# Kernel tuning notes

Hardware: AMD Instinct MI355X
Metric: run time of the kernel (lower is better)

Reference implementation:

```python
import jax, jax.numpy as jnp
import numpy as np

D = 1024
H = 16
HD = D // H
EPS = 1e-5

def _ln(t, gamma, beta):
    # LayerNorm over last dim (head_dim)
    mu = jnp.mean(t, axis=-1, keepdims=True)
    var = jnp.mean(jnp.square(t - mu), axis=-1, keepdims=True)
    return (t - mu) * jax.lax.rsqrt(var + EPS) * gamma + beta

def setup_inputs() -> dict:
    key = jax.random.key(0)
    ks = jax.random.split(key, 6)
    B, S = 2, 2048
    # xavier_uniform bound for square [D,D] weight
    bound = float(np.sqrt(6.0 / (D + D)))
    x = jax.random.normal(ks[0], (B, S, D), dtype=jnp.float32)
    Wq = jax.random.uniform(ks[1], (D, D), jnp.float32, -bound, bound)
    Wk = jax.random.uniform(ks[2], (D, D), jnp.float32, -bound, bound)
    Wv = jax.random.uniform(ks[3], (D, D), jnp.float32, -bound, bound)
    Wp = jax.random.uniform(ks[4], (D, D), jnp.float32, -bound, bound)
    bp = jnp.zeros((D,), jnp.float32)
    gq = jnp.ones((HD,), jnp.float32); bq = jnp.zeros((HD,), jnp.float32)
    gk = jnp.ones((HD,), jnp.float32); bk = jnp.zeros((HD,), jnp.float32)
    return {"x": x, "Wq": Wq, "Wk": Wk, "Wv": Wv, "Wp": Wp, "bp": bp,
            "gq": gq, "bq": bq, "gk": gk, "bk": bk}

def reference(x, Wq, Wk, Wv, Wp, bp, gq, bq, gk, bk):
    B, S, _ = x.shape
    scale = HD ** -0.5
    # torch Linear: x @ W.T -> (B,S,H,HD) -> (B,H,S,HD)
    q = (x @ Wq.T).reshape(B, S, H, HD).transpose(0, 2, 1, 3)
    k = (x @ Wk.T).reshape(B, S, H, HD).transpose(0, 2, 1, 3)
    v = (x @ Wv.T).reshape(B, S, H, HD).transpose(0, 2, 1, 3)
    q = _ln(q, gq, bq)
    k = _ln(k, gk, bk)
    scores = jnp.einsum('bhqd,bhkd->bhqk', q, k) * scale
    causal_mask = jnp.triu(jnp.ones((S, S), dtype=bool), k=1)  # True above diagonal
    scores = jnp.where(causal_mask[None, None], -jnp.inf, scores)
    attn = jax.nn.softmax(scores, axis=-1)
    out = jnp.einsum('bhqk,bhkd->bhqd', attn, v).transpose(0, 2, 1, 3).reshape(B, S, D)
    out = out @ Wp.T + bp
    return (out, attn)
```

## Files before the change

kernel.cpp:

```cpp
#include <hip/hip_runtime.h>

typedef _Float16 f16;
typedef _Float16 f16x4 __attribute__((ext_vector_type(4)));
typedef _Float16 f16x8 __attribute__((ext_vector_type(8)));
typedef float f32x4 __attribute__((ext_vector_type(4)));

#define D_ 1024
#define H_ 16
#define HD_ 64
#define B_ 2
#define S_ 2048
#define M_ 4096
#define SCALE 0.125f
#define NEG_BIG -1e30f

__device__ __forceinline__ float red16_sum(float v) {
#pragma unroll
  for (int m = 8; m >= 1; m >>= 1) v += __shfl_xor(v, m);
  return v;
}

__device__ __forceinline__ void gload16(const f16* g, f16* l) {
  __builtin_amdgcn_global_load_lds((const __attribute__((address_space(1))) void*)g,
                                   (__attribute__((address_space(3))) void*)l, 16, 0, 0);
}

__global__ __launch_bounds__(256) void k_cvt5(const float* __restrict__ x,
    const float* __restrict__ w0, const float* __restrict__ w1,
    const float* __restrict__ w2, const float* __restrict__ w3,
    f16* __restrict__ xh, f16* __restrict__ wh)
{
  const int y = blockIdx.y;
  const float* src; f16* dst; int n4;
  if (y == 0) { src = x; dst = xh; n4 = (M_ * D_) / 4; }
  else {
    src = (y == 1) ? w0 : (y == 2) ? w1 : (y == 3) ? w2 : w3;
    dst = wh + (size_t)(y - 1) * D_ * D_;
    n4 = (D_ * D_) / 4;
  }
  const int stride = gridDim.x * blockDim.x;
  for (int i = blockIdx.x * blockDim.x + threadIdx.x; i < n4; i += stride) {
    f32x4 v = ((const f32x4*)src)[i];
    ((f16x4*)dst)[i] = (f16x4){(f16)v[0], (f16)v[1], (f16)v[2], (f16)v[3]};
  }
}

__device__ __forceinline__ void gemm128(const f16* __restrict__ A, const f16* __restrict__ Bw,
                                        int K, int bm, int bn, f32x4 acc[4][4])
{
  __shared__ f16 As[128][64];
  __shared__ f16 Bs[128][64];
  const int tid = threadIdx.x;
  const int lane = tid & 63, wid = tid >> 6;
  const int wr = wid >> 1, wc = wid & 1, g = lane >> 4, li = lane & 15;
  const int lrow = lane >> 3, lcol = (lane & 7) * 8;

#pragma unroll
  for (int m = 0; m < 4; ++m)
#pragma unroll
    for (int n = 0; n < 4; ++n)
      acc[m][n] = (f32x4){0.f, 0.f, 0.f, 0.f};

  for (int k0 = 0; k0 < K; k0 += 64) {
#pragma unroll
    for (int i = 0; i < 4; ++i) {
      int c = wid * 4 + i;
      int row = c * 8 + lrow;
      gload16(&A[(size_t)(bm + row) * K + k0 + lcol], &As[c * 8][0]);
      gload16(&Bw[(size_t)(bn + row) * K + k0 + lcol], &Bs[c * 8][0]);
    }
    __syncthreads();
#pragma unroll
    for (int kk = 0; kk < 64; kk += 32) {
      f16x8 af[4], bf[4];
#pragma unroll
      for (int m = 0; m < 4; ++m) af[m] = *(const f16x8*)&As[wr * 64 + m * 16 + li][kk + g * 8];
#pragma unroll
      for (int n = 0; n < 4; ++n) bf[n] = *(const f16x8*)&Bs[wc * 64 + n * 16 + li][kk + g * 8];
#pragma unroll
      for (int m = 0; m < 4; ++m)
#pragma unroll
        for (int n = 0; n < 4; ++n)
          acc[m][n] = __builtin_amdgcn_mfma_f32_16x16x32_f16(af[m], bf[n], acc[m][n], 0, 0, 0);
    }
    __syncthreads();
  }
}

__global__ __launch_bounds__(256) void k_gemm_qkv(const f16* __restrict__ xh,
    const f16* __restrict__ wh,
    const float* __restrict__ gq, const float* __restrict__ bq,
    const float* __restrict__ gk, const float* __restrict__ bk,
    f16* __restrict__ qt, f16* __restrict__ kt, f16* __restrict__ vh)
{
  const int z = blockIdx.z;
  const f16* Bw = wh + (size_t)z * D_ * D_;
  f16* C = (z == 0) ? qt : (z == 1) ? kt : vh;
  f32x4 acc[4][4];
  gemm128(xh, Bw, D_, blockIdx.x * 128, blockIdx.y * 128, acc);
  const int tid = threadIdx.x, lane = tid & 63, wid = tid >> 6;
  const int wr = wid >> 1, wc = wid & 1, g = lane >> 4, li = lane & 15;
  const int hh = blockIdx.y * 2 + wc;
  const float* gamma = (z == 0) ? gq : gk;
  const float* beta  = (z == 0) ? bq : bk;
  float gm[4], bt[4];
  if (z < 2) {
#pragma unroll
    for (int n = 0; n < 4; ++n) { gm[n] = gamma[n * 16 + li]; bt[n] = beta[n * 16 + li]; }
  }
#pragma unroll
  for (int m = 0; m < 4; ++m)
#pragma unroll
    for (int r = 0; r < 4; ++r) {
      int rr = blockIdx.x * 128 + wr * 64 + m * 16 + g * 4 + r;
      int b = rr >> 11, s = rr & (S_ - 1);
      float v0 = acc[m][0][r], v1 = acc[m][1][r], v2 = acc[m][2][r], v3 = acc[m][3][r];
      if (z < 2) {
        float mean = red16_sum(v0 + v1 + v2 + v3) * (1.f / 64.f);
        v0 -= mean; v1 -= mean; v2 -= mean; v3 -= mean;
        float ss = red16_sum(v0 * v0 + v1 * v1 + v2 * v2 + v3 * v3);
        float inv = rsqrtf(ss * (1.f / 64.f) + 1e-5f);
        v0 = v0 * inv * gm[0] + bt[0]; v1 = v1 * inv * gm[1] + bt[1];
        v2 = v2 * inv * gm[2] + bt[2]; v3 = v3 * inv * gm[3] + bt[3];
      }
      f16* dst = C + ((size_t)(b * H_ + hh) * S_ + s) * HD_;
      dst[li]      = (f16)v0;
      dst[16 + li] = (f16)v1;
      dst[32 + li] = (f16)v2;
      dst[48 + li] = (f16)v3;
    }
}

__global__ __launch_bounds__(256) void k_gemm_proj(const f16* __restrict__ oh,
    const f16* __restrict__ Wph, const float* __restrict__ bp, float* __restrict__ out)
{
  f32x4 acc[4][4];
  gemm128(oh, Wph, D_, blockIdx.x * 128, blockIdx.y * 128, acc);
  const int tid = threadIdx.x, lane = tid & 63, wid = tid >> 6;
  const int wr = wid >> 1, wc = wid & 1, g = lane >> 4, li = lane & 15;
#pragma unroll
  for (int m = 0; m < 4; ++m)
#pragma unroll
    for (int n = 0; n < 4; ++n)
#pragma unroll
      for (int r = 0; r < 4; ++r) {
        int rr = blockIdx.x * 128 + wr * 64 + m * 16 + g * 4 + r;
        int cc = blockIdx.y * 128 + wc * 64 + n * 16 + li;
        out[(size_t)rr * D_ + cc] = acc[m][n][r] + bp[cc];
      }
}

__global__ __launch_bounds__(256) void k_transpose_v(const f16* __restrict__ vh, f16* __restrict__ vt)
{
  __shared__ f16 T[64][72];
  const int tid = threadIdx.x;
  const int s0 = blockIdx.x * 64, h = blockIdx.y, b = blockIdx.z;
  const f16* src = vh + ((size_t)(b * H_ + h) * S_ + s0) * HD_;
#pragma unroll
  for (int i = 0; i < 2; ++i) {
    int slot = tid + i * 256, sl = slot >> 3, ch = (slot & 7) * 8;
    *(f16x8*)&T[sl][ch] = *(const f16x8*)&src[(size_t)sl * HD_ + ch];
  }
  __syncthreads();
#pragma unroll
  for (int i = 0; i < 2; ++i) {
    int slot = tid + i * 256, d = slot >> 3, sc = (slot & 7) * 8;
    f16x8 val;
#pragma unroll
    for (int j = 0; j < 8; ++j) val[j] = T[sc + j][d];
    *(f16x8*)&vt[((size_t)(b * H_ + h) * HD_ + d) * S_ + s0 + sc] = val;
  }
}

__global__ __launch_bounds__(256, 4) void k_attn_stats(const f16* __restrict__ qt,
    const f16* __restrict__ kt, float* __restrict__ lpart)
{
  __shared__ float Ls[2][64];
  const int tq = 31 - blockIdx.x;
  const int ks = blockIdx.y;
  const int bh = blockIdx.z;
  const int tid = threadIdx.x, lane = tid & 63, wid = tid >> 6;
  const int wr = wid >> 1, wc = wid & 1, g = lane >> 4, li = lane & 15;
  const int ntk = (tq + 2) >> 1;
  const int t0 = ks * 8, t1 = (ntk < (ks + 1) * 8) ? ntk : (ks + 1) * 8;
  float* lp = lpart + ((size_t)(bh * 32 + tq) * 2 + ks) * 64;
  if (t0 >= t1) { if (tid < 64) lp[tid] = 0.f; return; }

  const f16* Qb = qt + (size_t)bh * S_ * HD_;
  const f16* Kb = kt + (size_t)bh * S_ * HD_;

  f16x8 qa[2][2];
#pragma unroll
  for (int m = 0; m < 2; ++m)
#pragma unroll
    for (int kk = 0; kk < 2; ++kk)
      qa[m][kk] = *(const f16x8*)&Qb[(size_t)(tq * 64 + wr * 32 + m * 16 + li) * HD_ + kk * 32 + g * 8];

  float lrun[2][4];
#pragma unroll
  for (int m = 0; m < 2; ++m)
#pragma unroll
    for (int r = 0; r < 4; ++r) lrun[m][r] = 0.f;

  for (int tk = t0; tk < t1; ++tk) {
    f32x4 acc[2][4];
#pragma unroll
    for (int m = 0; m < 2; ++m)
#pragma unroll
      for (int n = 0; n < 4; ++n) acc[m][n] = (f32x4){0.f, 0.f, 0.f, 0.f};
#pragma unroll
    for (int kk = 0; kk < 2; ++kk) {
      f16x8 kf[4];
#pragma unroll
      for (int n = 0; n < 4; ++n)
        kf[n] = *(const f16x8*)&Kb[(size_t)(tk * 128 + wc * 64 + n * 16 + li) * HD_ + kk * 32 + g * 8];
#pragma unroll
      for (int m = 0; m < 2; ++m)
#pragma unroll
        for (int n = 0; n < 4; ++n)
          acc[m][n] = __builtin_amdgcn_mfma_f32_16x16x32_f16(qa[m][kk], kf[n], acc[m][n], 0, 0, 0);
    }
    const bool diag = (tk == ntk - 1);
#pragma unroll
    for (int m = 0; m < 2; ++m)
#pragma unroll
      for (int r = 0; r < 4; ++r) {
        int row = tq * 64 + wr * 32 + m * 16 + g * 4 + r;
#pragma unroll
        for (int n = 0; n < 4; ++n) {
          float sv = acc[m][n][r] * SCALE;
          if (diag) { int col = tk * 128 + wc * 64 + n * 16 + li; if (col > row) sv = NEG_BIG; }
          lrun[m][r] += __expf(sv);
        }
      }
  }

#pragma unroll
  for (int m = 0; m < 2; ++m)
#pragma unroll
    for (int r = 0; r < 4; ++r) lrun[m][r] = red16_sum(lrun[m][r]);

  if (li == 0) {
#pragma unroll
    for (int m = 0; m < 2; ++m)
#pragma unroll
      for (int r = 0; r < 4; ++r)
        Ls[wc][wr * 32 + m * 16 + g * 4 + r] = lrun[m][r];
  }
  __syncthreads();
  if (tid < 64) lp[tid] = Ls[0][tid] + Ls[1][tid];
}

__global__ __launch_bounds__(256, 4) void k_attn_fused(const f16* __restrict__ qt,
    const f16* __restrict__ kt, const f16* __restrict__ vt,
    const float* __restrict__ lpart, float* __restrict__ attn, f16* __restrict__ oh)
{
  __shared__ f16 Ps[2][64][136];
  const int tq = 31 - blockIdx.x;
  const int bh = blockIdx.y, b = bh >> 4, h = bh & 15;
  const int tid = threadIdx.x, lane = tid & 63, wid = tid >> 6;
  const int wr = wid >> 1, wc = wid & 1, g = lane >> 4, li = lane & 15;
  const int ntk = (tq + 2) >> 1;
  const f16* Qb = qt + (size_t)bh * S_ * HD_;
  const f16* Kb = kt + (size_t)bh * S_ * HD_;
  float* attnB = attn + (size_t)bh * S_ * S_;
  const float* lp = lpart + (size_t)(bh * 32 + tq) * 2 * 64;

  f16x8 qa[2][2];
#pragma unroll
  for (int m = 0; m < 2; ++m)
#pragma unroll
    for (int kk = 0; kk < 2; ++kk)
      qa[m][kk] = *(const f16x8*)&Qb[(size_t)(tq * 64 + wr * 32 + m * 16 + li) * HD_ + kk * 32 + g * 8];
  float il[2][4];
#pragma unroll
  for (int m = 0; m < 2; ++m)
#pragma unroll
    for (int r = 0; r < 4; ++r) {
      int lr = wr * 32 + m * 16 + g * 4 + r;
      il[m][r] = 1.f / (lp[lr] + lp[64 + lr]);
    }

  f32x4 oacc[4];
#pragma unroll
  for (int n = 0; n < 4; ++n) oacc[n] = (f32x4){0.f, 0.f, 0.f, 0.f};

  const int r0 = tid >> 5, c0 = (tid & 31) * 4;
  int cur = 0;

  for (int tk = 0; tk < ntk; ++tk) {
    f32x4 acc[2][4];
#pragma unroll
    for (int m = 0; m < 2; ++m)
#pragma unroll
      for (int n = 0; n < 4; ++n) acc[m][n] = (f32x4){0.f, 0.f, 0.f, 0.f};
#pragma unroll
    for (int kk = 0; kk < 2; ++kk) {
      f16x8 kf[4];
#pragma unroll
      for (int n = 0; n < 4; ++n)
        kf[n] = *(const f16x8*)&Kb[(size_t)(tk * 128 + wc * 64 + n * 16 + li) * HD_ + kk * 32 + g * 8];
#pragma unroll
      for (int m = 0; m < 2; ++m)
#pragma unroll
        for (int n = 0; n < 4; ++n)
          acc[m][n] = __builtin_amdgcn_mfma_f32_16x16x32_f16(qa[m][kk], kf[n], acc[m][n], 0, 0, 0);
    }

    const bool diag = (tk == ntk - 1);
#pragma unroll
    for (int m = 0; m < 2; ++m)
#pragma unroll
      for (int r = 0; r < 4; ++r) {
        int row = tq * 64 + wr * 32 + m * 16 + g * 4 + r;
        float* rowp = attnB + (size_t)row * S_ + tk * 128 + wc * 64 + li;
#pragma unroll
        for (int n = 0; n < 4; ++n) {
          float sv = acc[m][n][r] * SCALE;
          if (diag) { int col = tk * 128 + wc * 64 + n * 16 + li; if (col > row) sv = NEG_BIG; }
          float p = __expf(sv) * il[m][r];
          __builtin_nontemporal_store(p, rowp + n * 16);
          Ps[cur][wr * 32 + m * 16 + g * 4 + r][wc * 64 + n * 16 + li] = (f16)p;
        }
      }
    __syncthreads();

#pragma unroll
    for (int kk = 0; kk < 4; ++kk) {
      f16x8 vbf[4];
#pragma unroll
      for (int n = 0; n < 4; ++n)
        vbf[n] = *(const f16x8*)&vt[((size_t)bh * HD_ + n * 16 + li) * S_ + tk * 128 + kk * 32 + g * 8];
      f16x8 pa = *(const f16x8*)&Ps[cur][wid * 16 + li][kk * 32 + g * 8];
#pragma unroll
      for (int n = 0; n < 4; ++n)
        oacc[n] = __builtin_amdgcn_mfma_f32_16x16x32_f16(pa, vbf[n], oacc[n], 0, 0, 0);
    }
    cur ^= 1;
  }

  for (int tk = ntk; tk < 16; ++tk) {
    float* arow0 = attnB + (size_t)(tq * 64) * S_ + tk * 128;
    f32x4 z = {0.f, 0.f, 0.f, 0.f};
#pragma unroll
    for (int rr = 0; rr < 64; rr += 8)
      __builtin_nontemporal_store(z, (f32x4*)(arow0 + (size_t)(rr + r0) * S_ + c0));
  }

#pragma unroll
  for (int n = 0; n < 4; ++n)
#pragma unroll
    for (int r = 0; r < 4; ++r) {
      int row = tq * 64 + wid * 16 + g * 4 + r;
      oh[(size_t)(b * S_ + row) * D_ + h * HD_ + n * 16 + li] = (f16)oacc[n][r];
    }
}

extern "C" void kernel_launch(void* const* d_in, const int* in_sizes, int n_in,
                              void* d_out, int out_size, void* d_ws, size_t ws_size,
                              hipStream_t stream)
{
  (void)in_sizes; (void)n_in; (void)out_size; (void)ws_size;
  const float* x  = (const float*)d_in[0];
  const float* Wq = (const float*)d_in[1];
  const float* Wk = (const float*)d_in[2];
  const float* Wv = (const float*)d_in[3];
  const float* Wp = (const float*)d_in[4];
  const float* bp = (const float*)d_in[5];
  const float* gq = (const float*)d_in[6];
  const float* bq = (const float*)d_in[7];
  const float* gk = (const float*)d_in[8];
  const float* bk = (const float*)d_in[9];

  float* out  = (float*)d_out;
  float* attn = out + (size_t)B_ * S_ * D_;

  f16* xh  = (f16*)d_ws;
  f16* wh  = xh + (size_t)M_ * D_;
  f16* qt  = wh + (size_t)4 * D_ * D_;
  f16* kt  = qt + (size_t)M_ * D_;
  f16* vh  = kt + (size_t)M_ * D_;
  f16* vt  = vh + (size_t)M_ * D_;
  f16* oh  = vt + (size_t)M_ * D_;
  float* lpart = (float*)(oh + (size_t)M_ * D_);

  dim3 blk(256);
  k_cvt5<<<dim3(256, 5), blk, 0, stream>>>(x, Wq, Wk, Wv, Wp, xh, wh);
  k_gemm_qkv<<<dim3(32, 8, 3), blk, 0, stream>>>(xh, wh, gq, bq, gk, bk, qt, kt, vh);
  k_transpose_v<<<dim3(32, 16, 2), blk, 0, stream>>>(vh, vt);
  k_attn_stats<<<dim3(32, 2, 32), blk, 0, stream>>>(qt, kt, lpart);
  k_attn_fused<<<dim3(32, 32), blk, 0, stream>>>(qt, kt, vt, lpart, attn, oh);
  k_gemm_proj<<<dim3(32, 8), blk, 0, stream>>>(oh, wh + (size_t)3 * D_ * D_, bp, out);
}
```

Before: 368.7 us.

## Split fused attention over two key ranges and merge partial outputs

The fused attention kernel's key-tile loop is now split into two halves along a new grid dimension, doubling the block count from 1024 to 2048 and evening out the causal load imbalance. Each half writes fp32 partial outputs to a workspace, and a new merge kernel sums them and converts to fp16 for the projection. This costs an extra launch plus extra global traffic for the partial buffers. The stats and V-transpose launches are also reordered.

```diff
diff --git a/kernel.cpp b/kernel.cpp
--- a/kernel.cpp
+++ b/kernel.cpp
@@ -253,14 +253,17 @@
 
 __global__ __launch_bounds__(256, 4) void k_attn_fused(const f16* __restrict__ qt,
     const f16* __restrict__ kt, const f16* __restrict__ vt,
-    const float* __restrict__ lpart, float* __restrict__ attn, f16* __restrict__ oh)
+    const float* __restrict__ lpart, float* __restrict__ attn, float* __restrict__ opart)
 {
   __shared__ f16 Ps[2][64][136];
   const int tq = 31 - blockIdx.x;
-  const int bh = blockIdx.y, b = bh >> 4, h = bh & 15;
+  const int ks = blockIdx.y;
+  const int bh = blockIdx.z;
   const int tid = threadIdx.x, lane = tid & 63, wid = tid >> 6;
   const int wr = wid >> 1, wc = wid & 1, g = lane >> 4, li = lane & 15;
   const int ntk = (tq + 2) >> 1;
+  const int t0 = ks * 8, t1 = t0 + 8;
+  const int c_end = (ntk < t1) ? ntk : t1;
   const f16* Qb = qt + (size_t)bh * S_ * HD_;
   const f16* Kb = kt + (size_t)bh * S_ * HD_;
   float* attnB = attn + (size_t)bh * S_ * S_;
@@ -288,7 +291,7 @@
   const int r0 = tid >> 5, c0 = (tid & 31) * 4;
   int cur = 0;
 
-  for (int tk = 0; tk < ntk; ++tk) {
+  for (int tk = t0; tk < c_end; ++tk) {
     f32x4 acc[2][4];
 #pragma unroll
     for (int m = 0; m < 2; ++m)
@@ -339,7 +342,8 @@
     cur ^= 1;
   }
 
-  for (int tk = ntk; tk < 16; ++tk) {
+  const int z0 = (ntk > t0) ? ntk : t0;
+  for (int tk = z0; tk < t1; ++tk) {
     float* arow0 = attnB + (size_t)(tq * 64) * S_ + tk * 128;
     f32x4 z = {0.f, 0.f, 0.f, 0.f};
 #pragma unroll
@@ -347,13 +351,27 @@
       __builtin_nontemporal_store(z, (f32x4*)(arow0 + (size_t)(rr + r0) * S_ + c0));
   }
 
+  float* op = opart + (((size_t)(ks * 32 + bh) * S_) + tq * 64) * HD_;
 #pragma unroll
   for (int n = 0; n < 4; ++n)
 #pragma unroll
-    for (int r = 0; r < 4; ++r) {
-      int row = tq * 64 + wid * 16 + g * 4 + r;
-      oh[(size_t)(b * S_ + row) * D_ + h * HD_ + n * 16 + li] = (f16)oacc[n][r];
-    }
+    for (int r = 0; r < 4; ++r)
+      op[(size_t)(wid * 16 + g * 4 + r) * HD_ + n * 16 + li] = oacc[n][r];
+}
+
+__global__ __launch_bounds__(256) void k_merge_o(const float* __restrict__ opart,
+                                                 f16* __restrict__ oh)
+{
+  int idx = blockIdx.x * 256 + threadIdx.x;
+  int hd4 = idx & 15;
+  int s   = (idx >> 4) & (S_ - 1);
+  int bh  = idx >> 15;
+  size_t src = ((size_t)bh * S_ + s) * HD_ + hd4 * 4;
+  f32x4 a = *(const f32x4*)&opart[src];
+  f32x4 c = *(const f32x4*)&opart[(size_t)32 * S_ * HD_ + src];
+  int b = bh >> 4, h = bh & 15;
+  f16x4 o = {(f16)(a[0] + c[0]), (f16)(a[1] + c[1]), (f16)(a[2] + c[2]), (f16)(a[3] + c[3])};
+  *(f16x4*)&oh[((size_t)(b * S_ + s)) * D_ + h * HD_ + hd4 * 4] = o;
 }
 
 extern "C" void kernel_launch(void* const* d_in, const int* in_sizes, int n_in,
@@ -383,12 +401,14 @@
   f16* vt  = vh + (size_t)M_ * D_;
   f16* oh  = vt + (size_t)M_ * D_;
   float* lpart = (float*)(oh + (size_t)M_ * D_);
+  float* opart = lpart + (size_t)32 * 32 * 2 * 64;
 
   dim3 blk(256);
   k_cvt5<<<dim3(256, 5), blk, 0, stream>>>(x, Wq, Wk, Wv, Wp, xh, wh);
   k_gemm_qkv<<<dim3(32, 8, 3), blk, 0, stream>>>(xh, wh, gq, bq, gk, bk, qt, kt, vh);
+  k_attn_stats<<<dim3(32, 2, 32), blk, 0, stream>>>(qt, kt, lpart);
   k_transpose_v<<<dim3(32, 16, 2), blk, 0, stream>>>(vh, vt);
-  k_attn_stats<<<dim3(32, 2, 32), blk, 0, stream>>>(qt, kt, lpart);
-  k_attn_fused<<<dim3(32, 32), blk, 0, stream>>>(qt, kt, vt, lpart, attn, oh);
+  k_attn_fused<<<dim3(32, 2, 32), blk, 0, stream>>>(qt, kt, vt, lpart, attn, opart);
+  k_merge_o<<<dim3(4096), blk, 0, stream>>>(opart, oh);
   k_gemm_proj<<<dim3(32, 8), blk, 0, stream>>>(oh, wh + (size_t)3 * D_ * D_, bp, out);
 }
```

Result: slower. 380.6 us (+3.2%).

## Split fused attention into single-wave 16-row blocks without block barriers

Applied to the files above, without the earlier changes.

The fused attention kernel now runs one 64-thread wave per block, each handling 16 query rows, across 4096 blocks instead of 1024 blocks of four waves. The P tile moves to a per-wave LDS buffer, which removes the __syncthreads and double buffering, and causal work is balanced at finer granularity. The cost is that K and V tiles are reused across only 16 rows rather than 64, so global/L2 traffic per output rises. The stats and V-transpose launches also swap order.

```diff
diff --git a/kernel.cpp b/kernel.cpp
--- a/kernel.cpp
+++ b/kernel.cpp
@@ -251,109 +251,100 @@
   if (tid < 64) lp[tid] = Ls[0][tid] + Ls[1][tid];
 }
 
-__global__ __launch_bounds__(256, 4) void k_attn_fused(const f16* __restrict__ qt,
+__global__ __launch_bounds__(64, 4) void k_attn_fused(const f16* __restrict__ qt,
     const f16* __restrict__ kt, const f16* __restrict__ vt,
     const float* __restrict__ lpart, float* __restrict__ attn, f16* __restrict__ oh)
 {
-  __shared__ f16 Ps[2][64][136];
-  const int tq = 31 - blockIdx.x;
-  const int bh = blockIdx.y, b = bh >> 4, h = bh & 15;
-  const int tid = threadIdx.x, lane = tid & 63, wid = tid >> 6;
-  const int wr = wid >> 1, wc = wid & 1, g = lane >> 4, li = lane & 15;
-  const int ntk = (tq + 2) >> 1;
+  __shared__ f16 Ps[16][138];
+  const int bx = blockIdx.x;
+  const int bh = bx & 31;
+  const int s  = 127 - (bx >> 5);
+  const int b = bh >> 4, h = bh & 15;
+  const int lane = threadIdx.x;
+  const int g = lane >> 4, li = lane & 15;
+  const int row0 = s * 16;
+  const int ntk = (s + 8) >> 3;
   const f16* Qb = qt + (size_t)bh * S_ * HD_;
   const f16* Kb = kt + (size_t)bh * S_ * HD_;
   float* attnB = attn + (size_t)bh * S_ * S_;
-  const float* lp = lpart + (size_t)(bh * 32 + tq) * 2 * 64;
-
-  f16x8 qa[2][2];
-#pragma unroll
-  for (int m = 0; m < 2; ++m)
-#pragma unroll
-    for (int kk = 0; kk < 2; ++kk)
-      qa[m][kk] = *(const f16x8*)&Qb[(size_t)(tq * 64 + wr * 32 + m * 16 + li) * HD_ + kk * 32 + g * 8];
-  float il[2][4];
-#pragma unroll
-  for (int m = 0; m < 2; ++m)
-#pragma unroll
-    for (int r = 0; r < 4; ++r) {
-      int lr = wr * 32 + m * 16 + g * 4 + r;
-      il[m][r] = 1.f / (lp[lr] + lp[64 + lr]);
-    }
+  const float* lp = lpart + (size_t)(bh * 32 + (s >> 2)) * 2 * 64;
+
+  f16x8 qa[2];
+#pragma unroll
+  for (int kk = 0; kk < 2; ++kk)
+    qa[kk] = *(const f16x8*)&Qb[(size_t)(row0 + li) * HD_ + kk * 32 + g * 8];
+
+  float il[4];
+#pragma unroll
+  for (int r = 0; r < 4; ++r) {
+    int lr = (s & 3) * 16 + g * 4 + r;
+    il[r] = 1.f / (lp[lr] + lp[64 + lr]);
+  }
 
   f32x4 oacc[4];
 #pragma unroll
   for (int n = 0; n < 4; ++n) oacc[n] = (f32x4){0.f, 0.f, 0.f, 0.f};
 
-  const int r0 = tid >> 5, c0 = (tid & 31) * 4;
-  int cur = 0;
-
   for (int tk = 0; tk < ntk; ++tk) {
-    f32x4 acc[2][4];
-#pragma unroll
-    for (int m = 0; m < 2; ++m)
-#pragma unroll
-      for (int n = 0; n < 4; ++n) acc[m][n] = (f32x4){0.f, 0.f, 0.f, 0.f};
-#pragma unroll
-    for (int kk = 0; kk < 2; ++kk) {
-      f16x8 kf[4];
-#pragma unroll
-      for (int n = 0; n < 4; ++n)
-        kf[n] = *(const f16x8*)&Kb[(size_t)(tk * 128 + wc * 64 + n * 16 + li) * HD_ + kk * 32 + g * 8];
-#pragma unroll
-      for (int m = 0; m < 2; ++m)
-#pragma unroll
-        for (int n = 0; n < 4; ++n)
-          acc[m][n] = __builtin_amdgcn_mfma_f32_16x16x32_f16(qa[m][kk], kf[n], acc[m][n], 0, 0, 0);
-    }
-
     const bool diag = (tk == ntk - 1);
 #pragma unroll
-    for (int m = 0; m < 2; ++m)
+    for (int nh = 0; nh < 2; ++nh) {
+      f32x4 acc[4];
+#pragma unroll
+      for (int j = 0; j < 4; ++j) acc[j] = (f32x4){0.f, 0.f, 0.f, 0.f};
+#pragma unroll
+      for (int kk = 0; kk < 2; ++kk) {
+        f16x8 kf[4];
+#pragma unroll
+        for (int j = 0; j < 4; ++j)
+          kf[j] = *(const f16x8*)&Kb[(size_t)(tk * 128 + nh * 64 + j * 16 + li) * HD_ + kk * 32 + g * 8];
+#pragma unroll
+        for (int j = 0; j < 4; ++j)
+          acc[j] = __builtin_amdgcn_mfma_f32_16x16x32_f16(qa[kk], kf[j], acc[j], 0, 0, 0);
+      }
 #pragma unroll
       for (int r = 0; r < 4; ++r) {
-        int row = tq * 64 + wr * 32 + m * 16 + g * 4 + r;
-        float* rowp = attnB + (size_t)row * S_ + tk * 128 + wc * 64 + li;
-#pragma unroll
-        for (int n = 0; n < 4; ++n) {
-          float sv = acc[m][n][r] * SCALE;
-          if (diag) { int col = tk * 128 + wc * 64 + n * 16 + li; if (col > row) sv = NEG_BIG; }
-          float p = __expf(sv) * il[m][r];
-          __builtin_nontemporal_store(p, rowp + n * 16);
-          Ps[cur][wr * 32 + m * 16 + g * 4 + r][wc * 64 + n * 16 + li] = (f16)p;
+        int row = row0 + g * 4 + r;
+        float* rowp = attnB + (size_t)row * S_ + tk * 128 + nh * 64 + li;
+#pragma unroll
+        for (int j = 0; j < 4; ++j) {
+          float sv = acc[j][r] * SCALE;
+          if (diag) { int col = tk * 128 + nh * 64 + j * 16 + li; if (col > row) sv = NEG_BIG; }
+          float p = __expf(sv) * il[r];
+          __builtin_nontemporal_store(p, rowp + j * 16);
+          Ps[g * 4 + r][nh * 64 + j * 16 + li] = (f16)p;
         }
       }
-    __syncthreads();
-
+    }
 #pragma unroll
     for (int kk = 0; kk < 4; ++kk) {
       f16x8 vbf[4];
 #pragma unroll
       for (int n = 0; n < 4; ++n)
         vbf[n] = *(const f16x8*)&vt[((size_t)bh * HD_ + n * 16 + li) * S_ + tk * 128 + kk * 32 + g * 8];
-      f16x8 pa = *(const f16x8*)&Ps[cur][wid * 16 + li][kk * 32 + g * 8];
+      f16x8 pa = *(const f16x8*)&Ps[li][kk * 32 + g * 8];
 #pragma unroll
       for (int n = 0; n < 4; ++n)
         oacc[n] = __builtin_amdgcn_mfma_f32_16x16x32_f16(pa, vbf[n], oacc[n], 0, 0, 0);
     }
-    cur ^= 1;
-  }
-
-  for (int tk = ntk; tk < 16; ++tk) {
-    float* arow0 = attnB + (size_t)(tq * 64) * S_ + tk * 128;
+  }
+
+  {
+    const int zr = lane >> 5, zc = (lane & 31) * 4;
     f32x4 z = {0.f, 0.f, 0.f, 0.f};
-#pragma unroll
-    for (int rr = 0; rr < 64; rr += 8)
-      __builtin_nontemporal_store(z, (f32x4*)(arow0 + (size_t)(rr + r0) * S_ + c0));
+    for (int tk = ntk; tk < 16; ++tk) {
+      float* a0 = attnB + (size_t)row0 * S_ + tk * 128;
+#pragma unroll
+      for (int rr = 0; rr < 16; rr += 2)
+        __builtin_nontemporal_store(z, (f32x4*)(a0 + (size_t)(rr + zr) * S_ + zc));
+    }
   }
 
 #pragma unroll
   for (int n = 0; n < 4; ++n)
 #pragma unroll
-    for (int r = 0; r < 4; ++r) {
-      int row = tq * 64 + wid * 16 + g * 4 + r;
-      oh[(size_t)(b * S_ + row) * D_ + h * HD_ + n * 16 + li] = (f16)oacc[n][r];
-    }
+    for (int r = 0; r < 4; ++r)
+      oh[(size_t)(b * S_ + row0 + g * 4 + r) * D_ + h * HD_ + n * 16 + li] = (f16)oacc[n][r];
 }
 
 extern "C" void kernel_launch(void* const* d_in, const int* in_sizes, int n_in,
@@ -387,8 +378,8 @@
   dim3 blk(256);
   k_cvt5<<<dim3(256, 5), blk, 0, stream>>>(x, Wq, Wk, Wv, Wp, xh, wh);
   k_gemm_qkv<<<dim3(32, 8, 3), blk, 0, stream>>>(xh, wh, gq, bq, gk, bk, qt, kt, vh);
+  k_attn_stats<<<dim3(32, 2, 32), blk, 0, stream>>>(qt, kt, lpart);
   k_transpose_v<<<dim3(32, 16, 2), blk, 0, stream>>>(vh, vt);
-  k_attn_stats<<<dim3(32, 2, 32), blk, 0, stream>>>(qt, kt, lpart);
-  k_attn_fused<<<dim3(32, 32), blk, 0, stream>>>(qt, kt, vt, lpart, attn, oh);
+  k_attn_fused<<<dim3(4096), dim3(64), 0, stream>>>(qt, kt, vt, lpart, attn, oh);
   k_gemm_proj<<<dim3(32, 8), blk, 0, stream>>>(oh, wh + (size_t)3 * D_ * D_, bp, out);
 }
```

Result: faster. 313.0 us (-15.1%).
